# Kernel tuning notes

Measured on AMD Instinct MI355X. Metric: run time of the kernel, lower is better.

The kernel has to match this reference:

```python
import jax, jax.numpy as jnp
import numpy as np

X_MIN, X_MAX = -3.0, 3.0
EPS = 1e-08


def setup_inputs() -> dict:
    key = jax.random.key(0)
    k1, k2, k3 = jax.random.split(key, 3)
    B, D_in, D_out, K = 8192, 512, 128, 16
    x = jax.random.normal(k1, (B, D_in), dtype=jnp.float32)
    # trunc_normal_(std=0.02) approximated by scaled normal
    weights = jax.random.normal(k2, (D_out, D_in, K), dtype=jnp.float32) * 0.02
    # xavier_uniform for skip
    limit = float(np.sqrt(6.0 / (D_in + D_out)))
    skip_w = jax.random.uniform(k3, (D_out, D_in), dtype=jnp.float32,
                                minval=-limit, maxval=limit)
    bias = jnp.zeros((D_out,), dtype=jnp.float32)
    return {"x": x, "weights": weights, "skip_w": skip_w, "bias": bias}


def reference(x, weights, skip_w, bias):
    # x: (B, D_in); weights: (D_out, D_in, K); skip_w: (D_out, D_in); bias: (D_out,)
    K = weights.shape[-1]
    t = jnp.clip((x - X_MIN) / (X_MAX - X_MIN + EPS), 0.0, 1.0)
    pos = t * (K - 1)
    idx0 = jnp.floor(pos).astype(jnp.int32)
    idx1 = jnp.minimum(idx0 + 1, K - 1)
    frac = jnp.clip(pos - idx0.astype(pos.dtype), 0.0, 1.0)
    # Hat-basis coefficients per (b, i): avoids materializing (B, D_out, D_in)
    oh0 = jax.nn.one_hot(idx0, K, dtype=x.dtype)  # (B, D_in, K)
    oh1 = jax.nn.one_hot(idx1, K, dtype=x.dtype)
    c = oh0 * (1.0 - frac)[..., None] + oh1 * frac[..., None]  # (B, D_in, K)
    # y[b,o] = sum_i (1-frac)*w[o,i,idx0] + frac*w[o,i,idx1]
    y = jnp.einsum('bik,oik->bo', c, weights)
    y = y + bias + x @ skip_w.T
    return y
```

## Files before the change

kernel.cpp:

```cpp
#include <hip/hip_runtime.h>

typedef __attribute__((ext_vector_type(8))) short short8;
typedef __attribute__((ext_vector_type(4))) float f32x4;

#define DIN 512
#define DOUT 128
#define KK 16
#define BTOT 8192
#define KAUG (DIN * KK + DIN)
#define NCHUNK_TOT (KAUG / 128)
#define NSPL 4
#define CPB (NCHUNK_TOT / NSPL)
#define BM 128
#define CHUNK_BYTES 32768
#define CT_BYTES 32768
#define CBASE 65536
#define LDS_BYTES 131072

__device__ static inline unsigned short f2bf(float x) {
  unsigned u = __builtin_bit_cast(unsigned, x);
  return (unsigned short)((u + 0x7FFFu + ((u >> 16) & 1u)) >> 16);
}

__device__ static inline void llds16(const char* g, char* l) {
  __builtin_amdgcn_global_load_lds(
      (const __attribute__((address_space(1))) unsigned int*)g,
      (__attribute__((address_space(3))) unsigned int*)l, 16, 0, 0);
}

__global__ __launch_bounds__(256) void build_wpp(const float* __restrict__ w,
                                                 const float* __restrict__ sk,
                                                 unsigned short* __restrict__ wpp) {
  const int gi = blockIdx.x * 256 + threadIdx.x;
  const int g = gi >> 11;
  const int rem = gi & 2047;
  const int o = rem >> 4;
  const int kcs = rem & 15;
  const int kc = kcs ^ (o & 15);
  const int kglob = g * 128 + kc * 8;
  const float* src = (kglob < 8192) ? (w + (size_t)o * 8192 + kglob)
                                    : (sk + (size_t)o * 512 + (kglob - 8192));
  const float4 v0 = ((const float4*)src)[0];
  const float4 v1 = ((const float4*)src)[1];
  uint4 pk;
  pk.x = f2bf(v0.x) | ((unsigned)f2bf(v0.y) << 16);
  pk.y = f2bf(v0.z) | ((unsigned)f2bf(v0.w) << 16);
  pk.z = f2bf(v1.x) | ((unsigned)f2bf(v1.y) << 16);
  pk.w = f2bf(v1.z) | ((unsigned)f2bf(v1.w) << 16);
  ((uint4*)wpp)[gi] = pk;
}

__global__ __launch_bounds__(512, 2) void kan_mfma(const float* __restrict__ x,
                                                   const unsigned short* __restrict__ wpp,
                                                   const float* __restrict__ bias,
                                                   float* __restrict__ out) {
  extern __shared__ __align__(16) char smem[];
  const int tid = threadIdx.x;
  const int bt = blockIdx.x >> 2;
  const int sp = blockIdx.x & 3;
  const int b0 = bt * BM;
  const int wid = tid >> 6, lane = tid & 63;
  const int lr = lane & 15, lq = lane >> 4;
  const int wm = wid >> 2, wn = wid & 3;
  const int g0 = sp * CPB;

  f32x4 acc[4][2] = {};

  auto stageW = [&](int g, int buf) {
    const char* gsrc = ((const char*)wpp) + (size_t)g * CHUNK_BYTES + wid * 4096 + lane * 16;
    char* ldst = smem + buf + wid * 4096;
#pragma unroll
    for (int it = 0; it < 4; ++it) llds16(gsrc + it * 1024, ldst + it * 1024);
  };

  auto buildSpline = [&](int cbuf, float xv0, float xv1) {
#pragma unroll
    for (int hh = 0; hh < 2; ++hh) {
      const int p = tid + hh * 512;
      const int bl = p >> 3, il = p & 7;
      const float xv = hh ? xv1 : xv0;
      float t = fminf(fmaxf((xv + 3.0f) * (1.0f / 6.0f), 0.0f), 1.0f);
      const float pos = t * 15.0f;
      int i0 = (int)pos;
      i0 = i0 > 14 ? 14 : i0;
      const float f = pos - (float)i0;
      char* row = smem + cbuf + bl * 256;
      const int swz = bl & 15;
      char* gA = row + (((il * 2) ^ swz) << 4);
      char* gB = row + (((il * 2 + 1) ^ swz) << 4);
      *(uint4*)gA = make_uint4(0, 0, 0, 0);
      *(uint4*)gB = make_uint4(0, 0, 0, 0);
      const unsigned short h0 = f2bf(1.0f - f);
      const unsigned short h1 = f2bf(f);
      const int i1 = i0 + 1;
      *(unsigned short*)(((i0 & 8) ? gB : gA) + (i0 & 7) * 2) = h0;
      *(unsigned short*)(((i1 & 8) ? gB : gA) + (i1 & 7) * 2) = h1;
    }
  };

  auto buildSkip = [&](int g, int cbuf) {
    const int ioff = (g - 64) * 128;
    const int bl = tid >> 2, q = tid & 3;
    const float* xr = x + (size_t)(b0 + bl) * DIN + ioff;
    char* row = smem + cbuf + bl * 256;
    const int swz = bl & 15;
#pragma unroll
    for (int gg = 0; gg < 4; ++gg) {
      const int kc = q * 4 + gg;
      const float4 v0 = ((const float4*)(xr + kc * 8))[0];
      const float4 v1 = ((const float4*)(xr + kc * 8))[1];
      uint4 pk;
      pk.x = f2bf(v0.x) | ((unsigned)f2bf(v0.y) << 16);
      pk.y = f2bf(v0.z) | ((unsigned)f2bf(v0.w) << 16);
      pk.z = f2bf(v1.x) | ((unsigned)f2bf(v1.y) << 16);
      pk.w = f2bf(v1.z) | ((unsigned)f2bf(v1.w) << 16);
      *(uint4*)(row + ((kc ^ swz) << 4)) = pk;
    }
  };

  auto loadX = [&](int g, float& a, float& b) {
    const int r0 = tid >> 3, il = tid & 7;
    a = x[(size_t)(b0 + r0) * DIN + g * 8 + il];
    b = x[(size_t)(b0 + 64 + r0) * DIN + g * 8 + il];
  };

  stageW(g0, 0);
  {
    float a, b;
    loadX(g0, a, b);
    buildSpline(CBASE + 0, a, b);
  }
  __syncthreads();

  for (int c = 0; c < CPB; ++c) {
    const int g = g0 + c;
    const int pb = (c & 1) << 15;
    const int nb = pb ^ 32768;
    const bool haveNext = (c + 1 < CPB);
    const int gn = g + 1;

    float xn0 = 0.0f, xn1 = 0.0f;
    if (haveNext && gn < 64) loadX(gn, xn0, xn1);
    if (haveNext) stageW(gn, nb);

    const char* Wb = smem + pb;
    const char* Cb = smem + CBASE + pb;
#pragma unroll
    for (int ks = 0; ks < 4; ++ks) {
      const int swq = ((ks * 4 + lq) ^ lr) << 4;
      short8 af[4], bfr[2];
#pragma unroll
      for (int mt = 0; mt < 4; ++mt)
        af[mt] = *(const short8*)(Cb + (wm * 64 + mt * 16 + lr) * 256 + swq);
#pragma unroll
      for (int nt = 0; nt < 2; ++nt)
        bfr[nt] = *(const short8*)(Wb + (wn * 32 + nt * 16 + lr) * 256 + swq);
#pragma unroll
      for (int mt = 0; mt < 4; ++mt)
#pragma unroll
        for (int nt = 0; nt < 2; ++nt)
          acc[mt][nt] = __builtin_amdgcn_mfma_f32_16x16x32_bf16(af[mt], bfr[nt], acc[mt][nt], 0, 0, 0);
    }

    if (haveNext) {
      if (gn < 64) buildSpline(CBASE + nb, xn0, xn1);
      else buildSkip(gn, CBASE + nb);
    }
    __syncthreads();
  }

#pragma unroll
  for (int nt = 0; nt < 2; ++nt) {
    const int col = wn * 32 + nt * 16 + lr;
    const float bv = (sp == 0) ? bias[col] : 0.0f;
#pragma unroll
    for (int mt = 0; mt < 4; ++mt) {
      const int rowb = b0 + wm * 64 + mt * 16 + lq * 4;
#pragma unroll
      for (int r = 0; r < 4; ++r)
        atomicAdd(out + (size_t)(rowb + r) * DOUT + col, acc[mt][nt][r] + bv);
    }
  }
}

__global__ void kan_naive(const float* __restrict__ x, const float* __restrict__ w,
                          const float* __restrict__ skw, const float* __restrict__ bias,
                          float* __restrict__ out) {
  const int b = blockIdx.x;
  const int o = threadIdx.x;
  float acc = bias[o];
  for (int i = 0; i < DIN; ++i) {
    float xv = x[(size_t)b * DIN + i];
    float t = fminf(fmaxf((xv + 3.0f) * (1.0f / 6.0f), 0.0f), 1.0f);
    float p = t * 15.0f;
    float fi = floorf(p);
    int i0 = (int)fi;
    int i1 = (i0 < 15) ? i0 + 1 : 15;
    float f = p - fi;
    const float* wr = &w[((size_t)o * DIN + i) * KK];
    acc += (1.0f - f) * wr[i0] + f * wr[i1] + xv * skw[(size_t)o * DIN + i];
  }
  out[(size_t)b * DOUT + o] = acc;
}

extern "C" void kernel_launch(void* const* d_in, const int* in_sizes, int n_in,
                              void* d_out, int out_size, void* d_ws, size_t ws_size,
                              hipStream_t stream) {
  const float* x    = (const float*)d_in[0];
  const float* w    = (const float*)d_in[1];
  const float* skw  = (const float*)d_in[2];
  const float* bias = (const float*)d_in[3];
  float* out = (float*)d_out;

  static bool lds_ok = []() {
    return hipFuncSetAttribute((const void*)kan_mfma,
                               hipFuncAttributeMaxDynamicSharedMemorySize,
                               LDS_BYTES) == hipSuccess;
  }();

  const size_t need = (size_t)NCHUNK_TOT * CHUNK_BYTES;
  if (ws_size < need || !lds_ok) {
    kan_naive<<<BTOT, DOUT, 0, stream>>>(x, w, skw, bias, out);
    return;
  }

  unsigned short* wpp = (unsigned short*)d_ws;

  hipMemsetAsync(d_out, 0, (size_t)out_size * sizeof(float), stream);
  build_wpp<<<NCHUNK_TOT * 2048 / 256, 256, 0, stream>>>(w, skw, wpp);
  kan_mfma<<<(BTOT / BM) * NSPL, 512, LDS_BYTES, stream>>>(x, wpp, bias, out);
}
```

Baseline: 110.2 us.

## Halve K-chunk to 64, use 4-wave blocks with 64x64 warp tiles, split-K 8

Shrinks the K chunk from 128 to 64 columns and halves LDS to a static 64 KB. Blocks drop from 8 to 4 waves, each wave now computing a 64x64 output tile for more MFMA reuse per LDS fragment load. The split-K factor doubles from 4 to 8, which gives more blocks but also twice as many atomic adds to the output. Weight prepacking and the XOR swizzle are rewritten for 128-byte rows.

```diff
diff --git a/kernel.cpp b/kernel.cpp
--- a/kernel.cpp
+++ b/kernel.cpp
@@ -8,14 +8,14 @@
 #define KK 16
 #define BTOT 8192
 #define KAUG (DIN * KK + DIN)
-#define NCHUNK_TOT (KAUG / 128)
-#define NSPL 4
+#define BK 64
+#define NCHUNK_TOT (KAUG / BK)
+#define NSPL 8
 #define CPB (NCHUNK_TOT / NSPL)
 #define BM 128
-#define CHUNK_BYTES 32768
-#define CT_BYTES 32768
-#define CBASE 65536
-#define LDS_BYTES 131072
+#define CHUNK_BYTES (DOUT * BK * 2)
+#define CBASE 32768
+#define LDS_BYTES 65536
 
 __device__ static inline unsigned short f2bf(float x) {
   unsigned u = __builtin_bit_cast(unsigned, x);
@@ -32,12 +32,12 @@
                                                  const float* __restrict__ sk,
                                                  unsigned short* __restrict__ wpp) {
   const int gi = blockIdx.x * 256 + threadIdx.x;
-  const int g = gi >> 11;
-  const int rem = gi & 2047;
-  const int o = rem >> 4;
-  const int kcs = rem & 15;
-  const int kc = kcs ^ (o & 15);
-  const int kglob = g * 128 + kc * 8;
+  const int g = gi >> 10;
+  const int rem = gi & 1023;
+  const int o = rem >> 3;
+  const int kcs = rem & 7;
+  const int kc = kcs ^ (o & 7);
+  const int kglob = g * 64 + kc * 8;
   const float* src = (kglob < 8192) ? (w + (size_t)o * 8192 + kglob)
                                     : (sk + (size_t)o * 512 + (kglob - 8192));
   const float4 v0 = ((const float4*)src)[0];
@@ -50,21 +50,21 @@
   ((uint4*)wpp)[gi] = pk;
 }
 
-__global__ __launch_bounds__(512, 2) void kan_mfma(const float* __restrict__ x,
+__global__ __launch_bounds__(256, 2) void kan_mfma(const float* __restrict__ x,
                                                    const unsigned short* __restrict__ wpp,
                                                    const float* __restrict__ bias,
                                                    float* __restrict__ out) {
-  extern __shared__ __align__(16) char smem[];
+  __shared__ __align__(16) char smem[LDS_BYTES];
   const int tid = threadIdx.x;
-  const int bt = blockIdx.x >> 2;
-  const int sp = blockIdx.x & 3;
+  const int bt = blockIdx.x >> 3;
+  const int sp = blockIdx.x & 7;
   const int b0 = bt * BM;
   const int wid = tid >> 6, lane = tid & 63;
   const int lr = lane & 15, lq = lane >> 4;
-  const int wm = wid >> 2, wn = wid & 3;
+  const int wm = wid >> 1, wn = wid & 1;
   const int g0 = sp * CPB;
 
-  f32x4 acc[4][2] = {};
+  f32x4 acc[4][4] = {};
 
   auto stageW = [&](int g, int buf) {
     const char* gsrc = ((const char*)wpp) + (size_t)g * CHUNK_BYTES + wid * 4096 + lane * 16;
@@ -76,16 +76,16 @@
   auto buildSpline = [&](int cbuf, float xv0, float xv1) {
 #pragma unroll
     for (int hh = 0; hh < 2; ++hh) {
-      const int p = tid + hh * 512;
-      const int bl = p >> 3, il = p & 7;
+      const int bl = (tid >> 2) + hh * 64;
+      const int il = tid & 3;
       const float xv = hh ? xv1 : xv0;
       float t = fminf(fmaxf((xv + 3.0f) * (1.0f / 6.0f), 0.0f), 1.0f);
       const float pos = t * 15.0f;
       int i0 = (int)pos;
       i0 = i0 > 14 ? 14 : i0;
       const float f = pos - (float)i0;
-      char* row = smem + cbuf + bl * 256;
-      const int swz = bl & 15;
+      char* row = smem + cbuf + bl * 128;
+      const int swz = bl & 7;
       char* gA = row + (((il * 2) ^ swz) << 4);
       char* gB = row + (((il * 2 + 1) ^ swz) << 4);
       *(uint4*)gA = make_uint4(0, 0, 0, 0);
@@ -99,11 +99,11 @@
   };
 
   auto buildSkip = [&](int g, int cbuf) {
-    const int ioff = (g - 64) * 128;
-    const int bl = tid >> 2, q = tid & 3;
+    const int ioff = (g - 128) * BK;
+    const int bl = tid >> 1, q = tid & 1;
     const float* xr = x + (size_t)(b0 + bl) * DIN + ioff;
-    char* row = smem + cbuf + bl * 256;
-    const int swz = bl & 15;
+    char* row = smem + cbuf + bl * 128;
+    const int swz = bl & 7;
 #pragma unroll
     for (int gg = 0; gg < 4; ++gg) {
       const int kc = q * 4 + gg;
@@ -119,9 +119,9 @@
   };
 
   auto loadX = [&](int g, float& a, float& b) {
-    const int r0 = tid >> 3, il = tid & 7;
-    a = x[(size_t)(b0 + r0) * DIN + g * 8 + il];
-    b = x[(size_t)(b0 + 64 + r0) * DIN + g * 8 + il];
+    const int r0 = tid >> 2, il = tid & 3;
+    a = x[(size_t)(b0 + r0) * DIN + g * 4 + il];
+    b = x[(size_t)(b0 + 64 + r0) * DIN + g * 4 + il];
   };
 
   stageW(g0, 0);
@@ -134,44 +134,48 @@
 
   for (int c = 0; c < CPB; ++c) {
     const int g = g0 + c;
-    const int pb = (c & 1) << 15;
-    const int nb = pb ^ 32768;
+    const int pb = (c & 1) << 14;
+    const int nb = pb ^ 16384;
     const bool haveNext = (c + 1 < CPB);
     const int gn = g + 1;
 
     float xn0 = 0.0f, xn1 = 0.0f;
-    if (haveNext && gn < 64) loadX(gn, xn0, xn1);
+    if (haveNext && gn < 128) loadX(gn, xn0, xn1);
     if (haveNext) stageW(gn, nb);
 
     const char* Wb = smem + pb;
     const char* Cb = smem + CBASE + pb;
 #pragma unroll
-    for (int ks = 0; ks < 4; ++ks) {
-      const int swq = ((ks * 4 + lq) ^ lr) << 4;
-      short8 af[4], bfr[2];
+    for (int ks = 0; ks < 2; ++ks) {
+      const int gq = ks * 4 + lq;
+      short8 af[4], bfr[4];
+#pragma unroll
+      for (int mt = 0; mt < 4; ++mt) {
+        const int m = wm * 64 + mt * 16 + lr;
+        af[mt] = *(const short8*)(Cb + m * 128 + ((gq ^ (m & 7)) << 4));
+      }
+#pragma unroll
+      for (int nt = 0; nt < 4; ++nt) {
+        const int o = wn * 64 + nt * 16 + lr;
+        bfr[nt] = *(const short8*)(Wb + o * 128 + ((gq ^ (o & 7)) << 4));
+      }
 #pragma unroll
       for (int mt = 0; mt < 4; ++mt)
-        af[mt] = *(const short8*)(Cb + (wm * 64 + mt * 16 + lr) * 256 + swq);
-#pragma unroll
-      for (int nt = 0; nt < 2; ++nt)
-        bfr[nt] = *(const short8*)(Wb + (wn * 32 + nt * 16 + lr) * 256 + swq);
-#pragma unroll
-      for (int mt = 0; mt < 4; ++mt)
-#pragma unroll
-        for (int nt = 0; nt < 2; ++nt)
+#pragma unroll
+        for (int nt = 0; nt < 4; ++nt)
           acc[mt][nt] = __builtin_amdgcn_mfma_f32_16x16x32_bf16(af[mt], bfr[nt], acc[mt][nt], 0, 0, 0);
     }
 
     if (haveNext) {
-      if (gn < 64) buildSpline(CBASE + nb, xn0, xn1);
+      if (gn < 128) buildSpline(CBASE + nb, xn0, xn1);
       else buildSkip(gn, CBASE + nb);
     }
     __syncthreads();
   }
 
 #pragma unroll
-  for (int nt = 0; nt < 2; ++nt) {
-    const int col = wn * 32 + nt * 16 + lr;
+  for (int nt = 0; nt < 4; ++nt) {
+    const int col = wn * 64 + nt * 16 + lr;
     const float bv = (sp == 0) ? bias[col] : 0.0f;
 #pragma unroll
     for (int mt = 0; mt < 4; ++mt) {
@@ -212,14 +216,8 @@
   const float* bias = (const float*)d_in[3];
   float* out = (float*)d_out;
 
-  static bool lds_ok = []() {
-    return hipFuncSetAttribute((const void*)kan_mfma,
-                               hipFuncAttributeMaxDynamicSharedMemorySize,
-                               LDS_BYTES) == hipSuccess;
-  }();
-
   const size_t need = (size_t)NCHUNK_TOT * CHUNK_BYTES;
-  if (ws_size < need || !lds_ok) {
+  if (ws_size < need) {
     kan_naive<<<BTOT, DOUT, 0, stream>>>(x, w, skw, bias, out);
     return;
   }
@@ -227,6 +225,6 @@
   unsigned short* wpp = (unsigned short*)d_ws;
 
   hipMemsetAsync(d_out, 0, (size_t)out_size * sizeof(float), stream);
-  build_wpp<<<NCHUNK_TOT * 2048 / 256, 256, 0, stream>>>(w, skw, wpp);
-  kan_mfma<<<(BTOT / BM) * NSPL, 512, LDS_BYTES, stream>>>(x, wpp, bias, out);
-}
+  build_wpp<<<NCHUNK_TOT * 1024 / 256, 256, 0, stream>>>(w, skw, wpp);
+  kan_mfma<<<(BTOT / BM) * NSPL, 256, 0, stream>>>(x, wpp, bias, out);
+}
```

After: 120.2 us. 9.1% more time.
